# Optimization experiments

Hardware: AMD Instinct MI355X
Metric: run time of the kernel (lower is better)

## Reference

```python
import jax, jax.numpy as jnp
import numpy as np

N = 500_000   # nodes
E = 8_000_000 # directed edges (before self-loops)


def _gcn_conv(x, src, dst, w, W, b):
    """PyG GCNConv: out = scatter_add(norm * (x @ W)[src] -> dst) + b,
    norm = deg^-1/2[src] * w * deg^-1/2[dst], deg from weighted in-edges at dst.
    src/dst/w already include self-loops."""
    h = x @ W                                                  # [N, out]
    deg = jax.ops.segment_sum(w, dst, num_segments=N)          # [N]
    dinv = jnp.where(deg > 0, jax.lax.rsqrt(deg), 0.0)
    norm = dinv[src] * w * dinv[dst]                           # [E+N]
    out = jax.ops.segment_sum(h[src] * norm[:, None], dst, num_segments=N)
    return out + b


def setup_inputs() -> dict:
    key = jax.random.key(0)
    ks = jax.random.split(key, 8)
    x = jax.random.normal(ks[0], (N, 4), dtype=jnp.float32)
    edge_index = jax.random.randint(ks[1], (2, E), 0, N, dtype=jnp.int64)
    edge_weight = jax.random.uniform(ks[2], (E,), dtype=jnp.float32)
    # Glorot-style params for conv1 (4->16) and conv2 (16->1)
    W1 = jax.random.normal(ks[3], (4, 16), dtype=jnp.float32) * (1.0 / np.sqrt(4))
    b1 = jnp.zeros((16,), dtype=jnp.float32)
    W2 = jax.random.normal(ks[4], (16, 1), dtype=jnp.float32) * (1.0 / np.sqrt(16))
    b2 = jnp.zeros((1,), dtype=jnp.float32)
    return {"x": x, "edge_index": edge_index, "edge_weight": edge_weight,
            "W1": W1, "b1": b1, "W2": W2, "b2": b2}


def reference(x, edge_index, edge_weight, W1, b1, W2, b2):
    # add self-loops with weight 1 (GCNConv default)
    loop = jnp.arange(N, dtype=edge_index.dtype)
    src = jnp.concatenate([edge_index[0], loop])
    dst = jnp.concatenate([edge_index[1], loop])
    w = jnp.concatenate([edge_weight, jnp.ones((N,), dtype=x.dtype)])
    h = jax.nn.relu(_gcn_conv(x, src, dst, w, W1, b1))   # [N, 16]
    out = _gcn_conv(h, src, dst, w, W2, b2)              # [N, 1]
    return out.reshape(-1)
```

## Files before the change

kernel.cpp:

```cpp
#include <hip/hip_runtime.h>
#include <hip/hip_fp16.h>


typedef unsigned long long u64;
typedef long long ll2 __attribute__((ext_vector_type(2)));

#define NPB_SHIFT 9
#define NPB 512
#define MAX_BINS 1024
#define PART_THREADS 1024
#define PART_EPT 16
#define PART_CHUNK (PART_THREADS * PART_EPT)
#define AGG_THREADS 512

#define Q11      2048.0f
#define INV11    (1.0f / 2048.0f)
#define A1_INV   (1.0f / 4194304.0f)
#define A2_INV   (1.0f / 1048576.0f)
#define BIAS     (1u << 25)
#define WQMASK   0x7FFu

struct h4 { __half2 a, b; };

__device__ __forceinline__ float4 h4_to_f4(h4 v) {
    float2 lo = __half22float2(v.a);
    float2 hi = __half22float2(v.b);
    return make_float4(lo.x, lo.y, hi.x, hi.y);
}

__global__ __launch_bounds__(1024)
void k_prep(const unsigned int* __restrict__ idx_words, int nCheck, int* flag,
            int* __restrict__ gCnt, int B, int nBlocks) {
    int gid = blockIdx.x * 1024 + threadIdx.x;
    for (int i = gid; i < B; i += nBlocks * 1024) gCnt[i] = 0;
    if (blockIdx.x == 0) {
        __shared__ int cnt;
        if (threadIdx.x == 0) cnt = 0;
        __syncthreads();
        int local = 0;
        for (int i = threadIdx.x; i < nCheck; i += 1024)
            local += (idx_words[2 * i + 1] != 0u) ? 1 : 0;
        if (local) atomicAdd(&cnt, local);
        __syncthreads();
        if (threadIdx.x == 0) *flag = (cnt < 8) ? 1 : 0;
    }
}

__global__ __launch_bounds__(PART_THREADS)
void k_partition(const void* __restrict__ idx, const float* __restrict__ ew,
                 int* __restrict__ gCnt, u64* __restrict__ slots,
                 int E, int B, int cap, const int* __restrict__ flag) {
    __shared__ int lcnt[MAX_BINS];
    __shared__ int lbase[MAX_BINS];
    __shared__ int lstart[MAX_BINS];
    __shared__ u64 sPay[PART_CHUNK];
    __shared__ int waveSum[PART_THREADS / 64];

    const bool is64 = (*flag != 0);
    const int tid = threadIdx.x;
    for (int i = tid; i < MAX_BINS; i += PART_THREADS) lcnt[i] = 0;
    __syncthreads();

    const int base_e = blockIdx.x * PART_CHUNK;
    const int nValid = min(PART_CHUNK, E - base_e);

    u64 pay[PART_EPT];
    int r_[PART_EPT];
#pragma unroll
    for (int i = 0; i < PART_EPT; ++i) {
        int e = base_e + i * PART_THREADS + tid;
        r_[i] = -1;
        if (e < E) {
            int s, d;
            if (is64) {
                const long long* p = (const long long*)idx;
                s = (int)__builtin_nontemporal_load(p + e);
                d = (int)__builtin_nontemporal_load(p + (long long)E + e);
            } else {
                const int* p = (const int*)idx;
                s = __builtin_nontemporal_load(p + e);
                d = __builtin_nontemporal_load(p + E + e);
            }
            float w = __builtin_nontemporal_load(ew + e);
            int bin = d >> NPB_SHIFT;
            unsigned wq = min((unsigned)__float2int_rn(w * Q11), 2047u);
            unsigned hi = ((unsigned)bin << 11) | wq;
            unsigned pk = ((unsigned)(d & (NPB - 1)) << 23) | (unsigned)s;
            pay[i] = ((u64)hi << 32) | pk;
            r_[i] = atomicAdd(&lcnt[bin], 1);
        }
    }
    __syncthreads();

    {
        const int lane = tid & 63, wid = tid >> 6;
        const int v = lcnt[tid];
        int inc = v;
#pragma unroll
        for (int off = 1; off < 64; off <<= 1) {
            int t = __shfl_up(inc, off, 64);
            if (lane >= off) inc += t;
        }
        if (lane == 63) waveSum[wid] = inc;
        __syncthreads();
        if (wid == 0) {
            const int NW = PART_THREADS / 64;
            int wv = (lane < NW) ? waveSum[lane] : 0;
            int winc = wv;
#pragma unroll
            for (int off = 1; off < NW; off <<= 1) {
                int t = __shfl_up(winc, off, 64);
                if (lane >= off) winc += t;
            }
            if (lane < NW) waveSum[lane] = winc - wv;
        }
        __syncthreads();
        lstart[tid] = inc - v + waveSum[wid];
        lbase[tid] = (v > 0 && tid < B) ? atomicAdd(&gCnt[tid], v) : 0;
    }
    __syncthreads();

#pragma unroll
    for (int i = 0; i < PART_EPT; ++i) {
        if (r_[i] >= 0) {
            int bin = (int)(pay[i] >> 43);
            sPay[lstart[bin] + r_[i]] = pay[i];
        }
    }
    __syncthreads();

    for (int k = tid; k < nValid; k += PART_THREADS) {
        u64 v = sPay[k];
        int bin = (int)(v >> 43);
        long long pos = (long long)lbase[bin] + (k - lstart[bin]);
        if (pos < cap) slots[(size_t)bin * cap + pos] = v;
    }
}

__device__ __forceinline__ void load4(const u64* __restrict__ sp, int j, int c,
                                      u64& v0, u64& v1, u64& v2, u64& v3) {
    v0 = v1 = v2 = v3 = 0;
    if (j + 3 < c) {
        ll2 q0 = *((const ll2*)(sp + j));
        ll2 q1 = *((const ll2*)(sp + j) + 1);
        v0 = (u64)q0.x; v1 = (u64)q0.y; v2 = (u64)q1.x; v3 = (u64)q1.y;
    } else if (j < c) {
        v0 = sp[j];
        if (j + 1 < c) v1 = sp[j + 1];
        if (j + 2 < c) v2 = sp[j + 2];
    }
}

__device__ __forceinline__ void load8(const u64* __restrict__ sp, int j, int c,
                                      u64* __restrict__ v) {
    if (j + 7 < c) {
#pragma unroll
        for (int q = 0; q < 4; ++q) {
            ll2 t = *((const ll2*)(sp + j) + q);
            v[2 * q]     = (u64)t.x;
            v[2 * q + 1] = (u64)t.y;
        }
    } else {
#pragma unroll
        for (int q = 0; q < 8; ++q)
            v[q] = (j + q < c) ? sp[j + q] : 0ULL;
    }
}

__global__ __launch_bounds__(AGG_THREADS, 8)
void k_deg_dinv(const u64* __restrict__ slots, const int* __restrict__ gCnt,
                const float4* __restrict__ x, float* __restrict__ dinv,
                h4* __restrict__ y, int* __restrict__ rowCnt, int N, int cap) {
    __shared__ unsigned degLds[NPB];
    const int b = blockIdx.x;
    for (int t = threadIdx.x; t < NPB; t += AGG_THREADS) degLds[t] = 0u;
    __syncthreads();
    const int c = min(gCnt[b], cap);
    const u64* sp = slots + (size_t)b * cap;
    const int CH = AGG_THREADS * 8;
    for (int base = 0; base < c; base += CH) {
        int j = base + (threadIdx.x << 3);
        u64 v[8];
        load8(sp, j, c, v);
#pragma unroll
        for (int q = 0; q < 8; ++q) {
            if (j + q < c)
                atomicAdd(&degLds[((unsigned)v[q]) >> 23],
                          (1u << 20) | ((unsigned)(v[q] >> 32) & WQMASK));
        }
    }
    __syncthreads();
    for (int t = threadIdx.x; t < NPB; t += AGG_THREADS) {
        int n = (b << NPB_SHIFT) + t;
        if (n < N) {
            unsigned dc = degLds[t];
            float di = rsqrtf(1.0f + (float)(dc & 0xFFFFFu) * INV11);
            dinv[n] = di;
            rowCnt[n] = (int)(dc >> 20);
            float4 xv = x[n];
            h4 hv;
            hv.a = __floats2half2_rn(xv.x * di, xv.y * di);
            hv.b = __floats2half2_rn(xv.z * di, xv.w * di);
            y[n] = hv;
        }
    }
}

__global__ __launch_bounds__(AGG_THREADS, 4)
void k_layer1(const u64* __restrict__ slots, const int* __restrict__ gCnt,
              const float* __restrict__ dinv, const h4* __restrict__ yh,
              const int* __restrict__ rowCnt, const float* __restrict__ W1,
              const float* __restrict__ b1, const float* __restrict__ W2,
              float* __restrict__ z, int N, int cap) {
    __shared__ u64 acc2[NPB][2];
    __shared__ float dLds[NPB];
    __shared__ float sW1[64], sb1[16], sW2[16];
    if (threadIdx.x < 64) sW1[threadIdx.x] = W1[threadIdx.x];
    if (threadIdx.x < 16) {
        sb1[threadIdx.x] = b1[threadIdx.x];
        sW2[threadIdx.x] = W2[threadIdx.x];
    }
    const int b = blockIdx.x;
    for (int t = threadIdx.x; t < NPB; t += AGG_THREADS) {
        acc2[t][0] = 0ULL; acc2[t][1] = 0ULL;
        int n = (b << NPB_SHIFT) + t;
        dLds[t] = (n < N) ? dinv[n] : 0.0f;
    }
    __syncthreads();
    const int c = min(gCnt[b], cap);
    const u64* sp = slots + (size_t)b * cap;
    const int CH = AGG_THREADS * 4;
    for (int base = 0; base < c; base += CH) {
        int j = base + (threadIdx.x << 2);
        u64 v0, v1, v2, v3;
        load4(sp, j, c, v0, v1, v2, v3);
        unsigned pk0 = (unsigned)v0, pk1 = (unsigned)v1,
                 pk2 = (unsigned)v2, pk3 = (unsigned)v3;
        float w0 = (float)((unsigned)(v0 >> 32) & WQMASK) * 2048.0f;
        float w1 = (float)((unsigned)(v1 >> 32) & WQMASK) * 2048.0f;
        float w2 = (float)((unsigned)(v2 >> 32) & WQMASK) * 2048.0f;
        float w3 = (float)((unsigned)(v3 >> 32) & WQMASK) * 2048.0f;
        h4 g0 = yh[pk0 & 0x7FFFFF];
        h4 g1 = yh[pk1 & 0x7FFFFF];
        h4 g2 = yh[pk2 & 0x7FFFFF];
        h4 g3 = yh[pk3 & 0x7FFFFF];
        float4 f0 = h4_to_f4(g0), f1 = h4_to_f4(g1),
               f2 = h4_to_f4(g2), f3 = h4_to_f4(g3);
        int d0 = pk0 >> 23, d1 = pk1 >> 23, d2 = pk2 >> 23, d3 = pk3 >> 23;
#define PACK2(wf, fa, fb) \
        (((u64)(unsigned)(__float2int_rn((wf) * (fb)) + (int)BIAS) << 32) | \
          (u64)(unsigned)(__float2int_rn((wf) * (fa)) + (int)BIAS))
        if (j < c) {
            atomicAdd(&acc2[d0][0], PACK2(w0, f0.x, f0.y));
            atomicAdd(&acc2[d0][1], PACK2(w0, f0.z, f0.w));
        }
        if (j + 1 < c) {
            atomicAdd(&acc2[d1][0], PACK2(w1, f1.x, f1.y));
            atomicAdd(&acc2[d1][1], PACK2(w1, f1.z, f1.w));
        }
        if (j + 2 < c) {
            atomicAdd(&acc2[d2][0], PACK2(w2, f2.x, f2.y));
            atomicAdd(&acc2[d2][1], PACK2(w2, f2.z, f2.w));
        }
        if (j + 3 < c) {
            atomicAdd(&acc2[d3][0], PACK2(w3, f3.x, f3.y));
            atomicAdd(&acc2[d3][1], PACK2(w3, f3.z, f3.w));
        }
#undef PACK2
    }
    __syncthreads();
    for (int t = threadIdx.x; t < NPB; t += AGG_THREADS) {
        int n = (b << NPB_SHIFT) + t;
        if (n >= N) continue;
        unsigned cb = (unsigned)rowCnt[n] * BIAS;
        u64 p01 = acc2[t][0], p23 = acc2[t][1];
        int a0 = (int)((unsigned)(p01 & 0xFFFFFFFFu) - cb);
        int a1 = (int)((unsigned)(p01 >> 32) - cb);
        int a2 = (int)((unsigned)(p23 & 0xFFFFFFFFu) - cb);
        int a3 = (int)((unsigned)(p23 >> 32) - cb);
        float di = dLds[t];
        float4 yv = h4_to_f4(yh[n]);
        float ax = di * (yv.x + (float)a0 * A1_INV);
        float ay = di * (yv.y + (float)a1 * A1_INV);
        float az = di * (yv.z + (float)a2 * A1_INV);
        float aw = di * (yv.w + (float)a3 * A1_INV);
        float sacc = 0.0f;
#pragma unroll
        for (int k = 0; k < 16; ++k) {
            float h = ax * sW1[k] + ay * sW1[16 + k] + az * sW1[32 + k]
                    + aw * sW1[48 + k] + sb1[k];
            sacc += fmaxf(h, 0.0f) * sW2[k];
        }
        z[n] = sacc * di;
    }
}

__global__ __launch_bounds__(AGG_THREADS, 8)
void k_layer2(const u64* __restrict__ slots, const int* __restrict__ gCnt,
              const float* __restrict__ dinv, const float* __restrict__ z,
              const float* __restrict__ b2, float* __restrict__ out,
              int N, int cap) {
    __shared__ int accs[NPB];
    __shared__ float dLds[NPB];
    const int b = blockIdx.x;
    for (int t = threadIdx.x; t < NPB; t += AGG_THREADS) {
        accs[t] = 0;
        int n = (b << NPB_SHIFT) + t;
        dLds[t] = (n < N) ? dinv[n] : 0.0f;
    }
    __syncthreads();
    const int c = min(gCnt[b], cap);
    const u64* sp = slots + (size_t)b * cap;
    const int CH = AGG_THREADS * 8;
    for (int base = 0; base < c; base += CH) {
        int j = base + (threadIdx.x << 3);
        u64 v[8];
        load8(sp, j, c, v);
        float zf[8];
#pragma unroll
        for (int q = 0; q < 8; ++q)
            zf[q] = z[(unsigned)v[q] & 0x7FFFFF];
#pragma unroll
        for (int q = 0; q < 8; ++q) {
            atomicAdd(&accs[((unsigned)v[q]) >> 23],
                      __float2int_rn((float)((unsigned)(v[q] >> 32) & WQMASK)
                                     * zf[q] * 512.0f));
        }
    }
    __syncthreads();
    const float bb2 = b2[0];
    for (int t = threadIdx.x; t < NPB; t += AGG_THREADS) {
        int n = (b << NPB_SHIFT) + t;
        if (n < N) out[n] = dLds[t] * (z[n] + (float)accs[t] * A2_INV) + bb2;
    }
}

__global__ __launch_bounds__(1024)
void k_detect(const unsigned int* __restrict__ idx_words, int nCheck, int* flag) {
    __shared__ int cnt;
    if (threadIdx.x == 0) cnt = 0;
    __syncthreads();
    int local = 0;
    for (int i = threadIdx.x; i < nCheck; i += blockDim.x)
        local += (idx_words[2 * i + 1] != 0u) ? 1 : 0;
    if (local) atomicAdd(&cnt, local);
    __syncthreads();
    if (threadIdx.x == 0) *flag = (cnt < 8) ? 1 : 0;
}

__global__ __launch_bounds__(256)
void k_init(float* __restrict__ deg, int N) {
    int i = blockIdx.x * blockDim.x + threadIdx.x;
    if (i < N) deg[i] = 1.0f;
}

__global__ __launch_bounds__(256)
void k_deg(const void* __restrict__ idx, const float* __restrict__ ew,
           float* __restrict__ deg, int E, const int* __restrict__ flag) {
    const bool is64 = (*flag != 0);
    const int stride = gridDim.x * blockDim.x;
    for (int e = blockIdx.x * blockDim.x + threadIdx.x; e < E; e += stride) {
        int d = is64 ? (int)((const long long*)idx)[(long long)E + e]
                     : ((const int*)idx)[E + e];
        atomicAdd(deg + d, ew[e]);
    }
}

__global__ __launch_bounds__(256)
void k_dinv_accx(float* __restrict__ deg_dinv, const float4* __restrict__ x,
                 float4* __restrict__ accx, int N) {
    int n = blockIdx.x * blockDim.x + threadIdx.x;
    if (n >= N) return;
    float dg = deg_dinv[n];
    float di = (dg > 0.0f) ? rsqrtf(dg) : 0.0f;
    deg_dinv[n] = di;
    float sn = di * di;
    float4 xv = x[n];
    accx[n] = make_float4(xv.x * sn, xv.y * sn, xv.z * sn, xv.w * sn);
}

__global__ __launch_bounds__(256)
void k_scatter1(const void* __restrict__ idx, const float* __restrict__ ew,
                const float* __restrict__ dinv, const float4* __restrict__ x,
                float* __restrict__ accx, int E, const int* __restrict__ flag) {
    const bool is64 = (*flag != 0);
    const int stride = gridDim.x * blockDim.x;
    for (int e = blockIdx.x * blockDim.x + threadIdx.x; e < E; e += stride) {
        int s, d;
        if (is64) {
            const long long* p = (const long long*)idx;
            s = (int)p[e]; d = (int)p[(long long)E + e];
        } else {
            const int* p = (const int*)idx;
            s = p[e]; d = p[E + e];
        }
        float nm = dinv[s] * ew[e] * dinv[d];
        float4 xv = x[s];
        float* dp = accx + (size_t)d * 4;
        atomicAdd(dp + 0, nm * xv.x);
        atomicAdd(dp + 1, nm * xv.y);
        atomicAdd(dp + 2, nm * xv.z);
        atomicAdd(dp + 3, nm * xv.w);
    }
}

__global__ __launch_bounds__(256)
void k_node2(const float4* __restrict__ accx, const float* __restrict__ dinv,
             const float* __restrict__ W1, const float* __restrict__ b1,
             const float* __restrict__ W2, const float* __restrict__ b2,
             float* __restrict__ s2, float* __restrict__ out, int N) {
    __shared__ float sW1[64], sb1[16], sW2[16];
    if (threadIdx.x < 64) sW1[threadIdx.x] = W1[threadIdx.x];
    if (threadIdx.x < 16) {
        sb1[threadIdx.x] = b1[threadIdx.x];
        sW2[threadIdx.x] = W2[threadIdx.x];
    }
    __syncthreads();
    int n = blockIdx.x * blockDim.x + threadIdx.x;
    if (n >= N) return;
    float bb2 = b2[0];
    float4 a = accx[n];
    float acc = 0.0f;
#pragma unroll
    for (int k = 0; k < 16; ++k) {
        float h = a.x * sW1[k] + a.y * sW1[16 + k] + a.z * sW1[32 + k]
                + a.w * sW1[48 + k] + sb1[k];
        acc += fmaxf(h, 0.0f) * sW2[k];
    }
    s2[n] = acc;
    float di = dinv[n];
    out[n] = acc * di * di + bb2;
}

__global__ __launch_bounds__(256)
void k_scatter2(const void* __restrict__ idx, const float* __restrict__ ew,
                const float* __restrict__ dinv, const float* __restrict__ s2,
                float* __restrict__ out, int E, const int* __restrict__ flag) {
    const bool is64 = (*flag != 0);
    const int stride = gridDim.x * blockDim.x;
    for (int e = blockIdx.x * blockDim.x + threadIdx.x; e < E; e += stride) {
        int s, d;
        if (is64) {
            const long long* p = (const long long*)idx;
            s = (int)p[e]; d = (int)p[(long long)E + e];
        } else {
            const int* p = (const int*)idx;
            s = p[e]; d = p[E + e];
        }
        float nm = dinv[s] * ew[e] * dinv[d];
        atomicAdd(out + d, nm * s2[s]);
    }
}

extern "C" void kernel_launch(void* const* d_in, const int* in_sizes, int n_in,
                              void* d_out, int out_size, void* d_ws, size_t ws_size,
                              hipStream_t stream) {
    const float* x   = (const float*)d_in[0];
    const void*  eix = d_in[1];
    const float* ew  = (const float*)d_in[2];
    const float* W1  = (const float*)d_in[3];
    const float* b1  = (const float*)d_in[4];
    const float* W2  = (const float*)d_in[5];
    const float* b2  = (const float*)d_in[6];
    float* out = (float*)d_out;

    const int N = in_sizes[0] / 4;
    const int E = in_sizes[2];

    const int B = (N + NPB - 1) >> NPB_SHIFT;
    int cap = (E / B + 2048 + 7) & ~7;
    const int nCheck = (E < 65536) ? E : 65536;

    size_t need = (size_t)N * 8 + (size_t)B * cap * 8
                + (size_t)B * 4 + (size_t)N * 12 + 256;

    bool addr32ok = ((long long)B * cap) < 0xFFFFFFFFLL;

    if (B <= MAX_BINS && N < (1 << 23) && ws_size >= need && addr32ok) {
        h4* y = (h4*)d_ws;
        u64* slots = (u64*)(y + N);
        int*   gCnt = (int*)(slots + (size_t)B * cap);
        int*   rowCnt = gCnt + B;
        float* dinv = (float*)(rowCnt + N);
        float* z    = dinv + N;
        int*   flag = (int*)(z + N);

        const int part_blocks = (E + PART_CHUNK - 1) / PART_CHUNK;

        k_prep<<<2, 1024, 0, stream>>>((const unsigned int*)eix, nCheck, flag,
                                       gCnt, B, 2);
        k_partition<<<part_blocks, PART_THREADS, 0, stream>>>(eix, ew, gCnt, slots,
                                                              E, B, cap, flag);
        k_deg_dinv<<<B, AGG_THREADS, 0, stream>>>(slots, gCnt, (const float4*)x,
                                                  dinv, y, rowCnt, N, cap);
        k_layer1<<<B, AGG_THREADS, 0, stream>>>(slots, gCnt, dinv, y, rowCnt,
                                                W1, b1, W2, z, N, cap);
        k_layer2<<<B, AGG_THREADS, 0, stream>>>(slots, gCnt, dinv, z, b2, out, N, cap);
    } else {
        const int nb_n = (N + 255) / 256;
        const int nb_e = min((E + 255) / 256, 16384);
        float* deg  = (float*)d_ws;
        float* accx = deg + N;
        float* s2   = accx + (size_t)4 * N;
        int*   flag = (int*)(s2 + N);

        k_init<<<nb_n, 256, 0, stream>>>(deg, N);
        k_detect<<<1, 1024, 0, stream>>>((const unsigned int*)eix, nCheck, flag);
        k_deg<<<nb_e, 256, 0, stream>>>(eix, ew, deg, E, flag);
        k_dinv_accx<<<nb_n, 256, 0, stream>>>(deg, (const float4*)x, (float4*)accx, N);
        k_scatter1<<<nb_e, 256, 0, stream>>>(eix, ew, deg, (const float4*)x, accx, E, flag);
        k_node2<<<nb_n, 256, 0, stream>>>((const float4*)accx, deg, W1, b1, W2, b2, s2, out, N);
        k_scatter2<<<nb_e, 256, 0, stream>>>(eix, ew, deg, s2, out, E, flag);
    }
}
```

Before: 179.2 us.

## Fuse degree and two aggregation passes into one cooperative kernel with grid syncs

Merges the degree/dinv, layer-1 and layer-2 bin kernels into a single cooperative kernel that loops over bins and separates the phases with grid-wide syncs. The grid is sized from the occupancy query and capped at 512 blocks. This removes two kernel launches and their inter-kernel gaps. In exchange each block processes several bins serially, occupancy is limited to 4 blocks per CU for all phases, and grid.sync adds barrier overhead. The old three-kernel path is kept as a fallback if the cooperative launch fails.

```diff
diff --git a/kernel.cpp b/kernel.cpp
--- a/kernel.cpp
+++ b/kernel.cpp
@@ -1,5 +1,8 @@
 #include <hip/hip_runtime.h>
 #include <hip/hip_fp16.h>
+#include <hip/hip_cooperative_groups.h>
+
+namespace cg = cooperative_groups;
 
 
 typedef unsigned long long u64;
@@ -12,6 +15,8 @@
 #define PART_EPT 16
 #define PART_CHUNK (PART_THREADS * PART_EPT)
 #define AGG_THREADS 512
+#define FUSE_THREADS 512
+#define FUSE_BLOCKS 512
 
 #define Q11      2048.0f
 #define INV11    (1.0f / 2048.0f)
@@ -167,17 +172,17 @@
     }
 }
 
-__global__ __launch_bounds__(AGG_THREADS, 8)
-void k_deg_dinv(const u64* __restrict__ slots, const int* __restrict__ gCnt,
-                const float4* __restrict__ x, float* __restrict__ dinv,
-                h4* __restrict__ y, int* __restrict__ rowCnt, int N, int cap) {
-    __shared__ unsigned degLds[NPB];
-    const int b = blockIdx.x;
-    for (int t = threadIdx.x; t < NPB; t += AGG_THREADS) degLds[t] = 0u;
+
+__device__ __forceinline__ void deg_body(
+        const u64* __restrict__ slots, const int* __restrict__ gCnt,
+        const float4* __restrict__ x, float* __restrict__ dinv,
+        h4* __restrict__ y, int* __restrict__ rowCnt, int N, int cap,
+        int b, unsigned* degLds, int nThreads) {
+    for (int t = threadIdx.x; t < NPB; t += nThreads) degLds[t] = 0u;
     __syncthreads();
     const int c = min(gCnt[b], cap);
     const u64* sp = slots + (size_t)b * cap;
-    const int CH = AGG_THREADS * 8;
+    const int CH = nThreads * 8;
     for (int base = 0; base < c; base += CH) {
         int j = base + (threadIdx.x << 3);
         u64 v[8];
@@ -190,7 +195,7 @@
         }
     }
     __syncthreads();
-    for (int t = threadIdx.x; t < NPB; t += AGG_THREADS) {
+    for (int t = threadIdx.x; t < NPB; t += nThreads) {
         int n = (b << NPB_SHIFT) + t;
         if (n < N) {
             unsigned dc = degLds[t];
@@ -204,24 +209,16 @@
             y[n] = hv;
         }
     }
-}
-
-__global__ __launch_bounds__(AGG_THREADS, 4)
-void k_layer1(const u64* __restrict__ slots, const int* __restrict__ gCnt,
-              const float* __restrict__ dinv, const h4* __restrict__ yh,
-              const int* __restrict__ rowCnt, const float* __restrict__ W1,
-              const float* __restrict__ b1, const float* __restrict__ W2,
-              float* __restrict__ z, int N, int cap) {
-    __shared__ u64 acc2[NPB][2];
-    __shared__ float dLds[NPB];
-    __shared__ float sW1[64], sb1[16], sW2[16];
-    if (threadIdx.x < 64) sW1[threadIdx.x] = W1[threadIdx.x];
-    if (threadIdx.x < 16) {
-        sb1[threadIdx.x] = b1[threadIdx.x];
-        sW2[threadIdx.x] = W2[threadIdx.x];
-    }
-    const int b = blockIdx.x;
-    for (int t = threadIdx.x; t < NPB; t += AGG_THREADS) {
+    __syncthreads();
+}
+
+__device__ __forceinline__ void layer1_body(
+        const u64* __restrict__ slots, const int* __restrict__ gCnt,
+        const float* __restrict__ dinv, const h4* __restrict__ yh,
+        const int* __restrict__ rowCnt, float* __restrict__ z, int N, int cap,
+        int b, u64 (*acc2)[2], float* dLds,
+        const float* sW1, const float* sb1, const float* sW2, int nThreads) {
+    for (int t = threadIdx.x; t < NPB; t += nThreads) {
         acc2[t][0] = 0ULL; acc2[t][1] = 0ULL;
         int n = (b << NPB_SHIFT) + t;
         dLds[t] = (n < N) ? dinv[n] : 0.0f;
@@ -229,7 +226,7 @@
     __syncthreads();
     const int c = min(gCnt[b], cap);
     const u64* sp = slots + (size_t)b * cap;
-    const int CH = AGG_THREADS * 4;
+    const int CH = nThreads * 4;
     for (int base = 0; base < c; base += CH) {
         int j = base + (threadIdx.x << 2);
         u64 v0, v1, v2, v3;
@@ -269,7 +266,7 @@
 #undef PACK2
     }
     __syncthreads();
-    for (int t = threadIdx.x; t < NPB; t += AGG_THREADS) {
+    for (int t = threadIdx.x; t < NPB; t += nThreads) {
         int n = (b << NPB_SHIFT) + t;
         if (n >= N) continue;
         unsigned cb = (unsigned)rowCnt[n] * BIAS;
@@ -293,6 +290,102 @@
         }
         z[n] = sacc * di;
     }
+    __syncthreads();
+}
+
+__device__ __forceinline__ void layer2_body(
+        const u64* __restrict__ slots, const int* __restrict__ gCnt,
+        const float* __restrict__ dinv, const float* __restrict__ z,
+        const float* __restrict__ b2, float* __restrict__ out, int N, int cap,
+        int b, int* accs, float* dLds, int nThreads) {
+    for (int t = threadIdx.x; t < NPB; t += nThreads) {
+        accs[t] = 0;
+        int n = (b << NPB_SHIFT) + t;
+        dLds[t] = (n < N) ? dinv[n] : 0.0f;
+    }
+    __syncthreads();
+    const int c = min(gCnt[b], cap);
+    const u64* sp = slots + (size_t)b * cap;
+    const int CH = nThreads * 8;
+    for (int base = 0; base < c; base += CH) {
+        int j = base + (threadIdx.x << 3);
+        u64 v[8];
+        load8(sp, j, c, v);
+        float zf[8];
+#pragma unroll
+        for (int q = 0; q < 8; ++q)
+            zf[q] = z[(unsigned)v[q] & 0x7FFFFF];
+#pragma unroll
+        for (int q = 0; q < 8; ++q) {
+            atomicAdd(&accs[((unsigned)v[q]) >> 23],
+                      __float2int_rn((float)((unsigned)(v[q] >> 32) & WQMASK)
+                                     * zf[q] * 512.0f));
+        }
+    }
+    __syncthreads();
+    const float bb2 = b2[0];
+    for (int t = threadIdx.x; t < NPB; t += nThreads) {
+        int n = (b << NPB_SHIFT) + t;
+        if (n < N) out[n] = dLds[t] * (z[n] + (float)accs[t] * A2_INV) + bb2;
+    }
+    __syncthreads();
+}
+
+__global__ __launch_bounds__(FUSE_THREADS, 4)
+void k_agg(const u64* __restrict__ slots, const int* __restrict__ gCnt,
+           const float4* __restrict__ x, const float* __restrict__ W1,
+           const float* __restrict__ b1, const float* __restrict__ W2,
+           const float* __restrict__ b2, float* __restrict__ dinv,
+           h4* __restrict__ y, int* __restrict__ rowCnt, float* __restrict__ z,
+           float* __restrict__ out, int N, int cap, int B) {
+    cg::grid_group grid = cg::this_grid();
+    __shared__ unsigned degLds[NPB];
+    __shared__ u64 acc2[NPB][2];
+    __shared__ float dLds[NPB];
+    __shared__ int accs[NPB];
+    __shared__ float sW1[64], sb1[16], sW2[16];
+    if (threadIdx.x < 64) sW1[threadIdx.x] = W1[threadIdx.x];
+    if (threadIdx.x < 16) {
+        sb1[threadIdx.x] = b1[threadIdx.x];
+        sW2[threadIdx.x] = W2[threadIdx.x];
+    }
+    for (int b = blockIdx.x; b < B; b += gridDim.x)
+        deg_body(slots, gCnt, x, dinv, y, rowCnt, N, cap, b, degLds, FUSE_THREADS);
+    grid.sync();
+    for (int b = blockIdx.x; b < B; b += gridDim.x)
+        layer1_body(slots, gCnt, dinv, (const h4*)y, rowCnt, z, N, cap, b,
+                    acc2, dLds, sW1, sb1, sW2, FUSE_THREADS);
+    grid.sync();
+    for (int b = blockIdx.x; b < B; b += gridDim.x)
+        layer2_body(slots, gCnt, dinv, z, b2, out, N, cap, b, accs, dLds,
+                    FUSE_THREADS);
+}
+
+__global__ __launch_bounds__(AGG_THREADS, 8)
+void k_deg_dinv(const u64* __restrict__ slots, const int* __restrict__ gCnt,
+                const float4* __restrict__ x, float* __restrict__ dinv,
+                h4* __restrict__ y, int* __restrict__ rowCnt, int N, int cap) {
+    __shared__ unsigned degLds[NPB];
+    deg_body(slots, gCnt, x, dinv, y, rowCnt, N, cap, blockIdx.x, degLds,
+             AGG_THREADS);
+}
+
+__global__ __launch_bounds__(AGG_THREADS, 4)
+void k_layer1(const u64* __restrict__ slots, const int* __restrict__ gCnt,
+              const float* __restrict__ dinv, const h4* __restrict__ yh,
+              const int* __restrict__ rowCnt, const float* __restrict__ W1,
+              const float* __restrict__ b1, const float* __restrict__ W2,
+              float* __restrict__ z, int N, int cap) {
+    __shared__ u64 acc2[NPB][2];
+    __shared__ float dLds[NPB];
+    __shared__ float sW1[64], sb1[16], sW2[16];
+    if (threadIdx.x < 64) sW1[threadIdx.x] = W1[threadIdx.x];
+    if (threadIdx.x < 16) {
+        sb1[threadIdx.x] = b1[threadIdx.x];
+        sW2[threadIdx.x] = W2[threadIdx.x];
+    }
+    layer1_body(slots, gCnt, dinv, yh, rowCnt, z, N, cap, blockIdx.x,
+                acc2, dLds, sW1, sb1, sW2, AGG_THREADS);
 }
 
 __global__ __launch_bounds__(AGG_THREADS, 8)
@@ -302,37 +395,8 @@
               int N, int cap) {
     __shared__ int accs[NPB];
     __shared__ float dLds[NPB];
-    const int b = blockIdx.x;
-    for (int t = threadIdx.x; t < NPB; t += AGG_THREADS) {
-        accs[t] = 0;
-        int n = (b << NPB_SHIFT) + t;
-        dLds[t] = (n < N) ? dinv[n] : 0.0f;
-    }
-    __syncthreads();
-    const int c = min(gCnt[b], cap);
-    const u64* sp = slots + (size_t)b * cap;
-    const int CH = AGG_THREADS * 8;
-    for (int base = 0; base < c; base += CH) {
-        int j = base + (threadIdx.x << 3);
-        u64 v[8];
-        load8(sp, j, c, v);
-        float zf[8];
-#pragma unroll
-        for (int q = 0; q < 8; ++q)
-            zf[q] = z[(unsigned)v[q] & 0x7FFFFF];
-#pragma unroll
-        for (int q = 0; q < 8; ++q) {
-            atomicAdd(&accs[((unsigned)v[q]) >> 23],
-                      __float2int_rn((float)((unsigned)(v[q] >> 32) & WQMASK)
-                                     * zf[q] * 512.0f));
-        }
-    }
-    __syncthreads();
-    const float bb2 = b2[0];
-    for (int t = threadIdx.x; t < NPB; t += AGG_THREADS) {
-        int n = (b << NPB_SHIFT) + t;
-        if (n < N) out[n] = dLds[t] * (z[n] + (float)accs[t] * A2_INV) + bb2;
-    }
+    layer2_body(slots, gCnt, dinv, z, b2, out, N, cap, blockIdx.x, accs, dLds,
+                AGG_THREADS);
 }
 
 __global__ __launch_bounds__(1024)
@@ -491,11 +555,33 @@
                                        gCnt, B, 2);
         k_partition<<<part_blocks, PART_THREADS, 0, stream>>>(eix, ew, gCnt, slots,
                                                               E, B, cap, flag);
-        k_deg_dinv<<<B, AGG_THREADS, 0, stream>>>(slots, gCnt, (const float4*)x,
-                                                  dinv, y, rowCnt, N, cap);
-        k_layer1<<<B, AGG_THREADS, 0, stream>>>(slots, gCnt, dinv, y, rowCnt,
-                                                W1, b1, W2, z, N, cap);
-        k_layer2<<<B, AGG_THREADS, 0, stream>>>(slots, gCnt, dinv, z, b2, out, N, cap);
+
+        const float4* x4 = (const float4*)x;
+        int Nv = N, capv = cap, Bv = B;
+        hipError_t cerr = hipErrorUnknown;
+        int maxPerCU = 0;
+        if (hipOccupancyMaxActiveBlocksPerMultiprocessor(&maxPerCU, k_agg,
+                                                         FUSE_THREADS, 0)
+                == hipSuccess && maxPerCU > 0) {
+            int fuseBlocks = maxPerCU * 256;
+            if (fuseBlocks > FUSE_BLOCKS) fuseBlocks = FUSE_BLOCKS;
+            if (fuseBlocks > B) fuseBlocks = B;
+            void* args[] = {(void*)&slots, (void*)&gCnt, (void*)&x4,
+                            (void*)&W1, (void*)&b1, (void*)&W2, (void*)&b2,
+                            (void*)&dinv, (void*)&y, (void*)&rowCnt,
+                            (void*)&z, (void*)&out,
+                            (void*)&Nv, (void*)&capv, (void*)&Bv};
+            cerr = hipLaunchCooperativeKernel((void*)k_agg, dim3(fuseBlocks),
+                                              dim3(FUSE_THREADS), args, 0, stream);
+        }
+        if (cerr != hipSuccess) {
+            k_deg_dinv<<<B, AGG_THREADS, 0, stream>>>(slots, gCnt, x4,
+                                                      dinv, y, rowCnt, N, cap);
+            k_layer1<<<B, AGG_THREADS, 0, stream>>>(slots, gCnt, dinv, y, rowCnt,
+                                                    W1, b1, W2, z, N, cap);
+            k_layer2<<<B, AGG_THREADS, 0, stream>>>(slots, gCnt, dinv, z, b2,
+                                                    out, N, cap);
+        }
     } else {
         const int nb_n = (N + 255) / 256;
         const int nb_e = min((E + 255) / 256, 16384);
```

Measured after the change: 265.8 us. 48.3% more time.
